# Performance work log

Hardware: AMD Instinct MI355X
Metric: run time of the kernel (lower is better)

Reference implementation:

```python
import jax, jax.numpy as jnp
import numpy as np

NUM_HEADS = 16
D_MODEL = 1024
D_KV = 64
NUM_BUCKETS = 32
MAX_DISTANCE = 128


def _relative_position_bucket(relative_position, num_buckets=NUM_BUCKETS, max_distance=MAX_DISTANCE):
    # faithful port of the torch static method (bidirectional variant)
    n = -relative_position
    nb = num_buckets // 2
    ret = (n < 0).astype(jnp.int32) * nb
    n = jnp.abs(n)
    max_exact = nb // 2
    is_small = n < max_exact
    # guard log(0); is_small branch covers n < max_exact anyway
    val_if_large = max_exact + (
        jnp.log(jnp.maximum(n, 1).astype(jnp.float32) / max_exact)
        / np.log(max_distance / max_exact)
        * (nb - max_exact)
    ).astype(jnp.int32)
    val_if_large = jnp.minimum(val_if_large, nb - 1)
    return ret + jnp.where(is_small, n, val_if_large)


def _compute_bias(seq_len, rel_bias):
    ctx = jnp.arange(seq_len)[:, None]
    mem = jnp.arange(seq_len)[None, :]
    bucket = _relative_position_bucket(mem - ctx)  # [S, S]
    values = rel_bias[bucket]                      # [S, S, H]
    return jnp.transpose(values, (2, 0, 1))[None]  # [1, H, S, S]


def setup_inputs() -> dict:
    key = jax.random.key(0)
    ks = jax.random.split(key, 6)
    B, S = 4, 1024
    scale = 1.0 / np.sqrt(D_MODEL)
    return {
        "hidden_states": jax.random.normal(ks[0], (B, S, D_MODEL), jnp.float32),
        "attention_mask": jnp.ones((B, 1, 1, S), jnp.int32),
        "Wq": jax.random.normal(ks[1], (NUM_HEADS * D_KV, D_MODEL), jnp.float32) * scale,
        "Wk": jax.random.normal(ks[2], (NUM_HEADS * D_KV, D_MODEL), jnp.float32) * scale,
        "Wv": jax.random.normal(ks[3], (NUM_HEADS * D_KV, D_MODEL), jnp.float32) * scale,
        "Wo": jax.random.normal(ks[4], (D_MODEL, NUM_HEADS * D_KV), jnp.float32) * scale,
        "rel_bias": jax.random.normal(ks[5], (NUM_BUCKETS, NUM_HEADS), jnp.float32),
    }


def reference(hidden_states, attention_mask, Wq, Wk, Wv, Wo, rel_bias):
    B, S, _ = hidden_states.shape
    # projections (Linear with bias=False: x @ W.T), reshape to [B, S, H, d_kv]
    q = jnp.einsum('bsd,ed->bse', hidden_states, Wq).reshape(B, S, NUM_HEADS, D_KV)
    k = jnp.einsum('bsd,ed->bse', hidden_states, Wk).reshape(B, S, NUM_HEADS, D_KV)
    v = jnp.einsum('bsd,ed->bse', hidden_states, Wv).reshape(B, S, NUM_HEADS, D_KV)
    scores = jnp.einsum('bqhd,bkhd->bhqk', q, k) / np.sqrt(D_KV)
    scores = scores + _compute_bias(S, rel_bias)
    scores = jnp.where(attention_mask == 0, jnp.float32(-1e9), scores)
    attn_weights = jax.nn.softmax(scores, axis=-1)  # dropout is identity at eval
    attn_output = jnp.einsum('bhqk,bkhd->bqhd', attn_weights, v).reshape(B, S, NUM_HEADS * D_KV)
    output = jnp.einsum('bse,de->bsd', attn_output, Wo)
    return output, attn_weights
```

## Files before the change

### kernel.cpp

```cpp
#include <hip/hip_runtime.h>
#include <hip/hip_bf16.h>

#define BB 4
#define SS 1024
#define HH 16
#define DK 64
#define DM 1024
#define MM (BB * SS)

typedef __attribute__((ext_vector_type(8))) short bh8_t;
typedef __attribute__((ext_vector_type(4))) float f4_t;

#define MFMA(a, b, c) __builtin_amdgcn_mfma_f32_16x16x32_bf16(a, b, c, 0, 0, 0)

__device__ __forceinline__ short f2bf(float f) {
    unsigned u = __builtin_bit_cast(unsigned, f);
    u = (u + 0x7FFFu + ((u >> 16) & 1u)) >> 16;
    return (short)u;
}
__device__ __forceinline__ float bf2f(short h) {
    unsigned u = ((unsigned)(unsigned short)h) << 16;
    return __builtin_bit_cast(float, u);
}

__device__ __forceinline__ int rel_bucket(int rel) {
    int n = -rel;
    int ret = 0;
    if (n < 0) { ret = 16; n = -n; }
    int v;
    if (n < 8) {
        v = n;
    } else {
        float t = logf((float)n * 0.125f) / 2.7725887298583984f * 8.0f;
        v = 8 + (int)t;
        if (v > 15) v = 15;
    }
    return ret + v;
}

__global__ __launch_bounds__(256)
void k_proj_qk(const float* __restrict__ X, const float* __restrict__ Wq,
               const float* __restrict__ Wk,
               short* __restrict__ Qh, short* __restrict__ Ql,
               short* __restrict__ Kh, short* __restrict__ Kl) {
    const int z = blockIdx.z;
    const float* W = z ? Wk : Wq;
    short* Oh = z ? Kh : Qh;
    short* Ol = z ? Kl : Ql;

    __shared__ short Ah[128][40], Al[128][40], Bh[128][40], Bl[128][40];

    const int tid = threadIdx.x;
    const int m0 = blockIdx.y * 128, n0 = blockIdx.x * 128;
    const int wave = tid >> 6, lane = tid & 63;
    const int quad = lane >> 4, lm = lane & 15;
    const int wm = (wave >> 1) * 64, wn = (wave & 1) * 64;
    const int r = tid >> 1, sg = (tid & 1) * 16;

    f4_t acc[4][4];
#pragma unroll
    for (int i = 0; i < 4; ++i)
#pragma unroll
        for (int j = 0; j < 4; ++j) acc[i][j] = (f4_t){0.f, 0.f, 0.f, 0.f};

    for (int k0 = 0; k0 < DM; k0 += 32) {
        f4_t xa[4], wb[4];
#pragma unroll
        for (int u = 0; u < 4; ++u) {
            xa[u] = *(const f4_t*)(X + (size_t)(m0 + r) * DM + k0 + sg + u * 4);
            wb[u] = *(const f4_t*)(W + (size_t)(n0 + r) * DM + k0 + sg + u * 4);
        }
        __syncthreads();
#pragma unroll
        for (int u = 0; u < 4; ++u) {
            short4 hh, ll;
            hh.x = f2bf(xa[u][0]); ll.x = f2bf(xa[u][0] - bf2f(hh.x));
            hh.y = f2bf(xa[u][1]); ll.y = f2bf(xa[u][1] - bf2f(hh.y));
            hh.z = f2bf(xa[u][2]); ll.z = f2bf(xa[u][2] - bf2f(hh.z));
            hh.w = f2bf(xa[u][3]); ll.w = f2bf(xa[u][3] - bf2f(hh.w));
            *(short4*)&Ah[r][sg + u * 4] = hh;
            *(short4*)&Al[r][sg + u * 4] = ll;
            hh.x = f2bf(wb[u][0]); ll.x = f2bf(wb[u][0] - bf2f(hh.x));
            hh.y = f2bf(wb[u][1]); ll.y = f2bf(wb[u][1] - bf2f(hh.y));
            hh.z = f2bf(wb[u][2]); ll.z = f2bf(wb[u][2] - bf2f(hh.z));
            hh.w = f2bf(wb[u][3]); ll.w = f2bf(wb[u][3] - bf2f(hh.w));
            *(short4*)&Bh[r][sg + u * 4] = hh;
            *(short4*)&Bl[r][sg + u * 4] = ll;
        }
        __syncthreads();

        bh8_t ah[4], al[4];
#pragma unroll
        for (int i = 0; i < 4; ++i) {
            ah[i] = *(const bh8_t*)&Ah[wm + i * 16 + lm][quad * 8];
            al[i] = *(const bh8_t*)&Al[wm + i * 16 + lm][quad * 8];
        }
#pragma unroll
        for (int j = 0; j < 4; ++j) {
            bh8_t bhj = *(const bh8_t*)&Bh[wn + j * 16 + lm][quad * 8];
            bh8_t blj = *(const bh8_t*)&Bl[wn + j * 16 + lm][quad * 8];
#pragma unroll
            for (int i = 0; i < 4; ++i) {
                acc[i][j] = MFMA(al[i], bhj, acc[i][j]);
                acc[i][j] = MFMA(ah[i], blj, acc[i][j]);
                acc[i][j] = MFMA(ah[i], bhj, acc[i][j]);
            }
        }
    }

#pragma unroll
    for (int i = 0; i < 4; ++i)
#pragma unroll
        for (int j = 0; j < 4; ++j)
#pragma unroll
            for (int g = 0; g < 4; ++g) {
                const int row = m0 + wm + i * 16 + quad * 4 + g;
                const int col = n0 + wn + j * 16 + lm;
                const int b = row >> 10, s = row & 1023;
                const int hd = col >> 6, dk = col & 63;
                const float v = acc[i][j][g];
                const short vh = f2bf(v);
                const short vl = f2bf(v - bf2f(vh));
                const size_t o = ((size_t)((b * HH + hd) * SS + s)) * DK + dk;
                Oh[o] = vh;
                Ol[o] = vl;
            }
}

__global__ __launch_bounds__(256)
void k_proj_v(const float* __restrict__ X, const float* __restrict__ Wv,
              short* __restrict__ Vt) {
    __shared__ short As[128][40], Bs[128][40];

    const int tid = threadIdx.x;
    const int m0 = blockIdx.y * 128, n0 = blockIdx.x * 128;
    const int wave = tid >> 6, lane = tid & 63;
    const int quad = lane >> 4, lm = lane & 15;
    const int wm = (wave >> 1) * 64, wn = (wave & 1) * 64;
    const int r = tid >> 1, sg = (tid & 1) * 16;

    f4_t acc[4][4];
#pragma unroll
    for (int i = 0; i < 4; ++i)
#pragma unroll
        for (int j = 0; j < 4; ++j) acc[i][j] = (f4_t){0.f, 0.f, 0.f, 0.f};

    for (int k0 = 0; k0 < DM; k0 += 32) {
        f4_t xa[4], wb[4];
#pragma unroll
        for (int u = 0; u < 4; ++u) {
            xa[u] = *(const f4_t*)(X + (size_t)(m0 + r) * DM + k0 + sg + u * 4);
            wb[u] = *(const f4_t*)(Wv + (size_t)(n0 + r) * DM + k0 + sg + u * 4);
        }
        __syncthreads();
#pragma unroll
        for (int u = 0; u < 4; ++u) {
            short4 hh;
            hh.x = f2bf(xa[u][0]); hh.y = f2bf(xa[u][1]);
            hh.z = f2bf(xa[u][2]); hh.w = f2bf(xa[u][3]);
            *(short4*)&As[r][sg + u * 4] = hh;
            hh.x = f2bf(wb[u][0]); hh.y = f2bf(wb[u][1]);
            hh.z = f2bf(wb[u][2]); hh.w = f2bf(wb[u][3]);
            *(short4*)&Bs[r][sg + u * 4] = hh;
        }
        __syncthreads();

        bh8_t ah[4];
#pragma unroll
        for (int i = 0; i < 4; ++i)
            ah[i] = *(const bh8_t*)&As[wm + i * 16 + lm][quad * 8];
#pragma unroll
        for (int j = 0; j < 4; ++j) {
            bh8_t bhj = *(const bh8_t*)&Bs[wn + j * 16 + lm][quad * 8];
#pragma unroll
            for (int i = 0; i < 4; ++i) acc[i][j] = MFMA(ah[i], bhj, acc[i][j]);
        }
    }

#pragma unroll
    for (int i = 0; i < 4; ++i)
#pragma unroll
        for (int j = 0; j < 4; ++j)
#pragma unroll
            for (int g = 0; g < 4; ++g) {
                const int row = m0 + wm + i * 16 + quad * 4 + g;
                const int col = n0 + wn + j * 16 + lm;
                const int b = row >> 10, s = row & 1023;
                const int hd = col >> 6, dk = col & 63;
                Vt[((size_t)((b * HH + hd) * DK + dk)) * SS + s] = f2bf(acc[i][j][g]);
            }
}

__global__ __launch_bounds__(256)
void k_scores(const short* __restrict__ Qh, const short* __restrict__ Ql,
              const short* __restrict__ Kh, const short* __restrict__ Kl,
              const int* __restrict__ mask, const float* __restrict__ rb,
              float* __restrict__ P) {
    __shared__ short Qhs[128][72], Qls[128][72], Khs[128][72], Kls[128][72];
    __shared__ float biasS[256];
    __shared__ int maskS[128];

    const int bh = blockIdx.z, b = bh >> 4, hd = bh & 15;
    const int q0 = blockIdx.y * 128, k0 = blockIdx.x * 128;
    const int tid = threadIdx.x;
    const int wave = tid >> 6, lane = tid & 63;
    const int quad = lane >> 4, lm = lane & 15;
    const int wm = (wave >> 1) * 64, wn = (wave & 1) * 64;

    {
        const int r = tid >> 1, sg = (tid & 1) * 32;
        const size_t qo = ((size_t)bh * SS + q0 + r) * DK + sg;
        const size_t ko = ((size_t)bh * SS + k0 + r) * DK + sg;
#pragma unroll
        for (int u = 0; u < 4; ++u) {
            *(uint4*)&Qhs[r][sg + u * 8] = *(const uint4*)(Qh + qo + u * 8);
            *(uint4*)&Qls[r][sg + u * 8] = *(const uint4*)(Ql + qo + u * 8);
            *(uint4*)&Khs[r][sg + u * 8] = *(const uint4*)(Kh + ko + u * 8);
            *(uint4*)&Kls[r][sg + u * 8] = *(const uint4*)(Kl + ko + u * 8);
        }
    }
    if (tid < 255) biasS[tid] = rb[rel_bucket(k0 - q0 + tid - 127) * HH + hd];
    if (tid < 128) maskS[tid] = mask[b * SS + k0 + tid];
    __syncthreads();

    f4_t acc[4][4];
#pragma unroll
    for (int i = 0; i < 4; ++i)
#pragma unroll
        for (int j = 0; j < 4; ++j) acc[i][j] = (f4_t){0.f, 0.f, 0.f, 0.f};

#pragma unroll
    for (int ks = 0; ks < 2; ++ks) {
        bh8_t ah[4], al[4];
#pragma unroll
        for (int i = 0; i < 4; ++i) {
            ah[i] = *(const bh8_t*)&Qhs[wm + i * 16 + lm][ks * 32 + quad * 8];
            al[i] = *(const bh8_t*)&Qls[wm + i * 16 + lm][ks * 32 + quad * 8];
        }
#pragma unroll
        for (int j = 0; j < 4; ++j) {
            bh8_t bhj = *(const bh8_t*)&Khs[wn + j * 16 + lm][ks * 32 + quad * 8];
            bh8_t blj = *(const bh8_t*)&Kls[wn + j * 16 + lm][ks * 32 + quad * 8];
#pragma unroll
            for (int i = 0; i < 4; ++i) {
                acc[i][j] = MFMA(al[i], bhj, acc[i][j]);
                acc[i][j] = MFMA(ah[i], blj, acc[i][j]);
                acc[i][j] = MFMA(ah[i], bhj, acc[i][j]);
            }
        }
    }

#pragma unroll
    for (int i = 0; i < 4; ++i)
#pragma unroll
        for (int j = 0; j < 4; ++j)
#pragma unroll
            for (int g = 0; g < 4; ++g) {
                const int rowl = wm + i * 16 + quad * 4 + g;
                const int coll = wn + j * 16 + lm;
                float s = acc[i][j][g] * 0.125f + biasS[coll - rowl + 127];
                s = (maskS[coll] == 0) ? -1e9f : s;
                P[((size_t)bh * SS + q0 + rowl) * SS + k0 + coll] = s;
            }
}

__global__ __launch_bounds__(256)
void k_softmax(float* __restrict__ P) {
    const size_t row = blockIdx.x;
    float4* p = reinterpret_cast<float4*>(P + row * 1024);
    const int tid = threadIdx.x;
    float4 v = p[tid];

    float m = fmaxf(fmaxf(v.x, v.y), fmaxf(v.z, v.w));
#pragma unroll
    for (int off = 32; off > 0; off >>= 1) m = fmaxf(m, __shfl_xor(m, off, 64));

    __shared__ float redm[4], reds[4];
    const int wave = tid >> 6, lane = tid & 63;
    if (lane == 0) redm[wave] = m;
    __syncthreads();
    m = fmaxf(fmaxf(redm[0], redm[1]), fmaxf(redm[2], redm[3]));

    const float e0 = expf(v.x - m), e1 = expf(v.y - m);
    const float e2 = expf(v.z - m), e3 = expf(v.w - m);
    float ssum = e0 + e1 + e2 + e3;
#pragma unroll
    for (int off = 32; off > 0; off >>= 1) ssum += __shfl_xor(ssum, off, 64);
    if (lane == 0) reds[wave] = ssum;
    __syncthreads();
    ssum = reds[0] + reds[1] + reds[2] + reds[3];

    const float inv = 1.0f / ssum;
    p[tid] = make_float4(e0 * inv, e1 * inv, e2 * inv, e3 * inv);
}

__global__ __launch_bounds__(256)
void k_pv(const float* __restrict__ P, const short* __restrict__ Vt,
          short* __restrict__ AO) {
    __shared__ short As[128][40];
    __shared__ short Bs[64][40];

    const int bh = blockIdx.y, b = bh >> 4, hd = bh & 15;
    const int q0 = blockIdx.x * 128;
    const int tid = threadIdx.x;
    const int wave = tid >> 6, lane = tid & 63;
    const int quad = lane >> 4, lm = lane & 15;
    const int wm = wave * 32;
    const int rA = tid >> 1, sgA = (tid & 1) * 16;
    const int rB = tid >> 2, sgB = (tid & 3) * 8;

    f4_t acc[2][4];
#pragma unroll
    for (int i = 0; i < 2; ++i)
#pragma unroll
        for (int j = 0; j < 4; ++j) acc[i][j] = (f4_t){0.f, 0.f, 0.f, 0.f};

    for (int k0 = 0; k0 < SS; k0 += 32) {
        f4_t pr[4];
#pragma unroll
        for (int u = 0; u < 4; ++u)
            pr[u] = *(const f4_t*)(P + ((size_t)bh * SS + q0 + rA) * SS + k0 + sgA + u * 4);
        uint4 vb = *(const uint4*)(Vt + ((size_t)bh * DK + rB) * SS + k0 + sgB);
        __syncthreads();
#pragma unroll
        for (int u = 0; u < 4; ++u) {
            short4 hh;
            hh.x = f2bf(pr[u][0]); hh.y = f2bf(pr[u][1]);
            hh.z = f2bf(pr[u][2]); hh.w = f2bf(pr[u][3]);
            *(short4*)&As[rA][sgA + u * 4] = hh;
        }
        *(uint4*)&Bs[rB][sgB] = vb;
        __syncthreads();

        bh8_t af0 = *(const bh8_t*)&As[wm + lm][quad * 8];
        bh8_t af1 = *(const bh8_t*)&As[wm + 16 + lm][quad * 8];
#pragma unroll
        for (int j = 0; j < 4; ++j) {
            bh8_t bf = *(const bh8_t*)&Bs[j * 16 + lm][quad * 8];
            acc[0][j] = MFMA(af0, bf, acc[0][j]);
            acc[1][j] = MFMA(af1, bf, acc[1][j]);
        }
    }

#pragma unroll
    for (int i = 0; i < 2; ++i)
#pragma unroll
        for (int j = 0; j < 4; ++j)
#pragma unroll
            for (int g = 0; g < 4; ++g) {
                const int s = q0 + wm + i * 16 + quad * 4 + g;
                const int dk = j * 16 + lm;
                AO[((size_t)(b * SS + s)) * DM + hd * DK + dk] = f2bf(acc[i][j][g]);
            }
}

__global__ __launch_bounds__(256)
void k_out(const short* __restrict__ A, const float* __restrict__ Wo,
           float* __restrict__ Out) {
    __shared__ short As[128][40], Bs[128][40];

    const int tid = threadIdx.x;
    const int m0 = blockIdx.y * 128, n0 = blockIdx.x * 128;
    const int wave = tid >> 6, lane = tid & 63;
    const int quad = lane >> 4, lm = lane & 15;
    const int wm = (wave >> 1) * 64, wn = (wave & 1) * 64;
    const int r = tid >> 1, sg = (tid & 1) * 16;

    f4_t acc[4][4];
#pragma unroll
    for (int i = 0; i < 4; ++i)
#pragma unroll
        for (int j = 0; j < 4; ++j) acc[i][j] = (f4_t){0.f, 0.f, 0.f, 0.f};

    for (int k0 = 0; k0 < DM; k0 += 32) {
        uint4 a0 = *(const uint4*)(A + (size_t)(m0 + r) * DM + k0 + sg);
        uint4 a1 = *(const uint4*)(A + (size_t)(m0 + r) * DM + k0 + sg + 8);
        f4_t wb[4];
#pragma unroll
        for (int u = 0; u < 4; ++u)
            wb[u] = *(const f4_t*)(Wo + (size_t)(n0 + r) * DM + k0 + sg + u * 4);
        __syncthreads();
        *(uint4*)&As[r][sg] = a0;
        *(uint4*)&As[r][sg + 8] = a1;
#pragma unroll
        for (int u = 0; u < 4; ++u) {
            short4 hh;
            hh.x = f2bf(wb[u][0]); hh.y = f2bf(wb[u][1]);
            hh.z = f2bf(wb[u][2]); hh.w = f2bf(wb[u][3]);
            *(short4*)&Bs[r][sg + u * 4] = hh;
        }
        __syncthreads();

        bh8_t ah[4];
#pragma unroll
        for (int i = 0; i < 4; ++i)
            ah[i] = *(const bh8_t*)&As[wm + i * 16 + lm][quad * 8];
#pragma unroll
        for (int j = 0; j < 4; ++j) {
            bh8_t bhj = *(const bh8_t*)&Bs[wn + j * 16 + lm][quad * 8];
#pragma unroll
            for (int i = 0; i < 4; ++i) acc[i][j] = MFMA(ah[i], bhj, acc[i][j]);
        }
    }

#pragma unroll
    for (int i = 0; i < 4; ++i)
#pragma unroll
        for (int j = 0; j < 4; ++j)
#pragma unroll
            for (int g = 0; g < 4; ++g)
                Out[(size_t)(m0 + wm + i * 16 + quad * 4 + g) * DM + n0 + wn + j * 16 + lm] =
                    acc[i][j][g];
}

extern "C" void kernel_launch(void* const* d_in, const int* in_sizes, int n_in,
                              void* d_out, int out_size, void* d_ws, size_t ws_size,
                              hipStream_t stream) {
    const float* X    = (const float*)d_in[0];
    const int*   mask = (const int*)d_in[1];
    const float* Wq   = (const float*)d_in[2];
    const float* Wk   = (const float*)d_in[3];
    const float* Wv   = (const float*)d_in[4];
    const float* Wo   = (const float*)d_in[5];
    const float* rb   = (const float*)d_in[6];

    float* out = (float*)d_out;
    float* P   = out + (size_t)BB * SS * DM;

    short* ws = (short*)d_ws;
    short* Qh = ws;
    short* Ql = ws + (size_t)4194304;
    short* Kh = ws + (size_t)8388608;
    short* Kl = ws + (size_t)12582912;
    short* Vt = ws + (size_t)16777216;
    short* AO = ws;

    k_proj_qk<<<dim3(8, 32, 2), 256, 0, stream>>>(X, Wq, Wk, Qh, Ql, Kh, Kl);
    k_proj_v <<<dim3(8, 32, 1), 256, 0, stream>>>(X, Wv, Vt);
    k_scores <<<dim3(8, 8, BB * HH), 256, 0, stream>>>(Qh, Ql, Kh, Kl, mask, rb, P);
    k_softmax<<<dim3(BB * HH * SS), 256, 0, stream>>>(P);
    k_pv     <<<dim3(8, BB * HH), 256, 0, stream>>>(P, Vt, AO);
    k_out    <<<dim3(8, 32), 256, 0, stream>>>(AO, Wo, out);
}
```

Before: 659.2 us.

## Pre-convert inputs to bf16 once and fuse scores with softmax

Adds a conversion kernel that turns X and all weights into bf16 hi/lo splits once, so the projection and output GEMMs load ready-made bf16 tiles instead of converting fp32 inside every K-loop. It also merges the score and softmax kernels: each block computes a full 16x1024 row strip of scores and normalises it in registers before writing P. This drops one full write-and-read of the 256 MB score matrix, at the cost of larger workspace traffic for the converted copies and lower per-block reuse of Q.

```diff
diff --git a/kernel.cpp b/kernel.cpp
--- a/kernel.cpp
+++ b/kernel.cpp
@@ -39,12 +39,44 @@
 }
 
 __global__ __launch_bounds__(256)
-void k_proj_qk(const float* __restrict__ X, const float* __restrict__ Wq,
-               const float* __restrict__ Wk,
+void k_cvt(const float* __restrict__ X, const float* __restrict__ Wq,
+           const float* __restrict__ Wk, const float* __restrict__ Wv,
+           const float* __restrict__ Wo,
+           short* __restrict__ Xh, short* __restrict__ Xl,
+           short* __restrict__ Wqh, short* __restrict__ Wql,
+           short* __restrict__ Wkh, short* __restrict__ Wkl,
+           short* __restrict__ Wvh, short* __restrict__ Woh) {
+    const long base = ((long)blockIdx.x * 256 + threadIdx.x) * 4;
+    const float* src;
+    short* dh;
+    short* dl = nullptr;
+    long off;
+    if (base < 4194304L)      { src = X;  dh = Xh;  dl = Xl;  off = base; }
+    else if (base < 5242880L) { src = Wq; dh = Wqh; dl = Wql; off = base - 4194304L; }
+    else if (base < 6291456L) { src = Wk; dh = Wkh; dl = Wkl; off = base - 5242880L; }
+    else if (base < 7340032L) { src = Wv; dh = Wvh;           off = base - 6291456L; }
+    else                      { src = Wo; dh = Woh;           off = base - 7340032L; }
+    float4 v = *(const float4*)(src + off);
+    short4 h;
+    h.x = f2bf(v.x); h.y = f2bf(v.y); h.z = f2bf(v.z); h.w = f2bf(v.w);
+    *(short4*)(dh + off) = h;
+    if (dl) {
+        short4 l;
+        l.x = f2bf(v.x - bf2f(h.x)); l.y = f2bf(v.y - bf2f(h.y));
+        l.z = f2bf(v.z - bf2f(h.z)); l.w = f2bf(v.w - bf2f(h.w));
+        *(short4*)(dl + off) = l;
+    }
+}
+
+__global__ __launch_bounds__(256)
+void k_proj_qk(const short* __restrict__ Xh, const short* __restrict__ Xl,
+               const short* __restrict__ Wqh, const short* __restrict__ Wql,
+               const short* __restrict__ Wkh, const short* __restrict__ Wkl,
                short* __restrict__ Qh, short* __restrict__ Ql,
                short* __restrict__ Kh, short* __restrict__ Kl) {
     const int z = blockIdx.z;
-    const float* W = z ? Wk : Wq;
+    const short* Wh_ = z ? Wkh : Wqh;
+    const short* Wl_ = z ? Wkl : Wql;
     short* Oh = z ? Kh : Qh;
     short* Ol = z ? Kl : Ql;
 
@@ -64,29 +96,17 @@
         for (int j = 0; j < 4; ++j) acc[i][j] = (f4_t){0.f, 0.f, 0.f, 0.f};
 
     for (int k0 = 0; k0 < DM; k0 += 32) {
-        f4_t xa[4], wb[4];
-#pragma unroll
-        for (int u = 0; u < 4; ++u) {
-            xa[u] = *(const f4_t*)(X + (size_t)(m0 + r) * DM + k0 + sg + u * 4);
-            wb[u] = *(const f4_t*)(W + (size_t)(n0 + r) * DM + k0 + sg + u * 4);
-        }
-        __syncthreads();
-#pragma unroll
-        for (int u = 0; u < 4; ++u) {
-            short4 hh, ll;
-            hh.x = f2bf(xa[u][0]); ll.x = f2bf(xa[u][0] - bf2f(hh.x));
-            hh.y = f2bf(xa[u][1]); ll.y = f2bf(xa[u][1] - bf2f(hh.y));
-            hh.z = f2bf(xa[u][2]); ll.z = f2bf(xa[u][2] - bf2f(hh.z));
-            hh.w = f2bf(xa[u][3]); ll.w = f2bf(xa[u][3] - bf2f(hh.w));
-            *(short4*)&Ah[r][sg + u * 4] = hh;
-            *(short4*)&Al[r][sg + u * 4] = ll;
-            hh.x = f2bf(wb[u][0]); ll.x = f2bf(wb[u][0] - bf2f(hh.x));
-            hh.y = f2bf(wb[u][1]); ll.y = f2bf(wb[u][1] - bf2f(hh.y));
-            hh.z = f2bf(wb[u][2]); ll.z = f2bf(wb[u][2] - bf2f(hh.z));
-            hh.w = f2bf(wb[u][3]); ll.w = f2bf(wb[u][3] - bf2f(hh.w));
-            *(short4*)&Bh[r][sg + u * 4] = hh;
-            *(short4*)&Bl[r][sg + u * 4] = ll;
-        }
+        const size_t ao = (size_t)(m0 + r) * DM + k0 + sg;
+        const size_t bo = (size_t)(n0 + r) * DM + k0 + sg;
+        uint4 ah0 = *(const uint4*)(Xh + ao), ah1 = *(const uint4*)(Xh + ao + 8);
+        uint4 al0 = *(const uint4*)(Xl + ao), al1 = *(const uint4*)(Xl + ao + 8);
+        uint4 bh0 = *(const uint4*)(Wh_ + bo), bh1 = *(const uint4*)(Wh_ + bo + 8);
+        uint4 bl0 = *(const uint4*)(Wl_ + bo), bl1 = *(const uint4*)(Wl_ + bo + 8);
+        __syncthreads();
+        *(uint4*)&Ah[r][sg] = ah0; *(uint4*)&Ah[r][sg + 8] = ah1;
+        *(uint4*)&Al[r][sg] = al0; *(uint4*)&Al[r][sg + 8] = al1;
+        *(uint4*)&Bh[r][sg] = bh0; *(uint4*)&Bh[r][sg + 8] = bh1;
+        *(uint4*)&Bl[r][sg] = bl0; *(uint4*)&Bl[r][sg + 8] = bl1;
         __syncthreads();
 
         bh8_t ah[4], al[4];
@@ -128,7 +148,7 @@
 }
 
 __global__ __launch_bounds__(256)
-void k_proj_v(const float* __restrict__ X, const float* __restrict__ Wv,
+void k_proj_v(const short* __restrict__ Xh, const short* __restrict__ Wvh,
               short* __restrict__ Vt) {
     __shared__ short As[128][40], Bs[128][40];
 
@@ -146,23 +166,13 @@
         for (int j = 0; j < 4; ++j) acc[i][j] = (f4_t){0.f, 0.f, 0.f, 0.f};
 
     for (int k0 = 0; k0 < DM; k0 += 32) {
-        f4_t xa[4], wb[4];
-#pragma unroll
-        for (int u = 0; u < 4; ++u) {
-            xa[u] = *(const f4_t*)(X + (size_t)(m0 + r) * DM + k0 + sg + u * 4);
-            wb[u] = *(const f4_t*)(Wv + (size_t)(n0 + r) * DM + k0 + sg + u * 4);
-        }
-        __syncthreads();
-#pragma unroll
-        for (int u = 0; u < 4; ++u) {
-            short4 hh;
-            hh.x = f2bf(xa[u][0]); hh.y = f2bf(xa[u][1]);
-            hh.z = f2bf(xa[u][2]); hh.w = f2bf(xa[u][3]);
-            *(short4*)&As[r][sg + u * 4] = hh;
-            hh.x = f2bf(wb[u][0]); hh.y = f2bf(wb[u][1]);
-            hh.z = f2bf(wb[u][2]); hh.w = f2bf(wb[u][3]);
-            *(short4*)&Bs[r][sg + u * 4] = hh;
-        }
+        const size_t ao = (size_t)(m0 + r) * DM + k0 + sg;
+        const size_t bo = (size_t)(n0 + r) * DM + k0 + sg;
+        uint4 a0 = *(const uint4*)(Xh + ao), a1 = *(const uint4*)(Xh + ao + 8);
+        uint4 b0 = *(const uint4*)(Wvh + bo), b1 = *(const uint4*)(Wvh + bo + 8);
+        __syncthreads();
+        *(uint4*)&As[r][sg] = a0; *(uint4*)&As[r][sg + 8] = a1;
+        *(uint4*)&Bs[r][sg] = b0; *(uint4*)&Bs[r][sg + 8] = b1;
         __syncthreads();
 
         bh8_t ah[4];
@@ -192,106 +202,141 @@
 }
 
 __global__ __launch_bounds__(256)
-void k_scores(const short* __restrict__ Qh, const short* __restrict__ Ql,
-              const short* __restrict__ Kh, const short* __restrict__ Kl,
-              const int* __restrict__ mask, const float* __restrict__ rb,
-              float* __restrict__ P) {
-    __shared__ short Qhs[128][72], Qls[128][72], Khs[128][72], Kls[128][72];
-    __shared__ float biasS[256];
-    __shared__ int maskS[128];
-
-    const int bh = blockIdx.z, b = bh >> 4, hd = bh & 15;
-    const int q0 = blockIdx.y * 128, k0 = blockIdx.x * 128;
+void k_ssm(const short* __restrict__ Qh, const short* __restrict__ Ql,
+           const short* __restrict__ Kh, const short* __restrict__ Kl,
+           const int* __restrict__ mask, const float* __restrict__ rb,
+           float* __restrict__ P) {
+    __shared__ short Qhs[16][72], Qls[16][72];
+    __shared__ short Khs[128][72], Kls[128][72];
+    __shared__ float biasS[1040];
+    __shared__ int maskS[1024];
+    __shared__ float red[4][16];
+
+    const int bh = blockIdx.y, b = bh >> 4, h = bh & 15;
+    const int q0 = blockIdx.x * 16;
     const int tid = threadIdx.x;
     const int wave = tid >> 6, lane = tid & 63;
     const int quad = lane >> 4, lm = lane & 15;
-    const int wm = (wave >> 1) * 64, wn = (wave & 1) * 64;
-
-    {
-        const int r = tid >> 1, sg = (tid & 1) * 32;
+
+    if (tid < 128) {
+        const int r = tid >> 3, sg = (tid & 7) * 8;
         const size_t qo = ((size_t)bh * SS + q0 + r) * DK + sg;
-        const size_t ko = ((size_t)bh * SS + k0 + r) * DK + sg;
+        *(uint4*)&Qhs[r][sg] = *(const uint4*)(Qh + qo);
+        *(uint4*)&Qls[r][sg] = *(const uint4*)(Ql + qo);
+    }
+    for (int i = tid; i < 1039; i += 256)
+        biasS[i] = rb[rel_bucket(i - 15 - q0) * HH + h];
+    *(int4*)&maskS[tid * 4] = *(const int4*)(mask + b * SS + tid * 4);
+    __syncthreads();
+
+    bh8_t qh[2], ql[2];
+#pragma unroll
+    for (int ks = 0; ks < 2; ++ks) {
+        qh[ks] = *(const bh8_t*)&Qhs[lm][ks * 32 + quad * 8];
+        ql[ks] = *(const bh8_t*)&Qls[lm][ks * 32 + quad * 8];
+    }
+
+    f4_t acc[16];
+#pragma unroll
+    for (int i = 0; i < 16; ++i) acc[i] = (f4_t){0.f, 0.f, 0.f, 0.f};
+
+    const int rK = tid >> 1, sgK = (tid & 1) * 32;
+#pragma unroll
+    for (int c = 0; c < 8; ++c) {
+        const int kc = c * 128;
+        uint4 vh[4], vl[4];
+        const size_t ko = ((size_t)bh * SS + kc + rK) * DK + sgK;
 #pragma unroll
         for (int u = 0; u < 4; ++u) {
-            *(uint4*)&Qhs[r][sg + u * 8] = *(const uint4*)(Qh + qo + u * 8);
-            *(uint4*)&Qls[r][sg + u * 8] = *(const uint4*)(Ql + qo + u * 8);
-            *(uint4*)&Khs[r][sg + u * 8] = *(const uint4*)(Kh + ko + u * 8);
-            *(uint4*)&Kls[r][sg + u * 8] = *(const uint4*)(Kl + ko + u * 8);
-        }
-    }
-    if (tid < 255) biasS[tid] = rb[rel_bucket(k0 - q0 + tid - 127) * HH + hd];
-    if (tid < 128) maskS[tid] = mask[b * SS + k0 + tid];
+            vh[u] = *(const uint4*)(Kh + ko + u * 8);
+            vl[u] = *(const uint4*)(Kl + ko + u * 8);
+        }
+        __syncthreads();
+#pragma unroll
+        for (int u = 0; u < 4; ++u) {
+            *(uint4*)&Khs[rK][sgK + u * 8] = vh[u];
+            *(uint4*)&Kls[rK][sgK + u * 8] = vl[u];
+        }
+        __syncthreads();
+
+#pragma unroll
+        for (int t = 0; t < 2; ++t) {
+            const int col0 = wave * 32 + t * 16;
+            const int ai = c * 2 + t;
+#pragma unroll
+            for (int ks = 0; ks < 2; ++ks) {
+                bh8_t kbh = *(const bh8_t*)&Khs[col0 + lm][ks * 32 + quad * 8];
+                bh8_t kbl = *(const bh8_t*)&Kls[col0 + lm][ks * 32 + quad * 8];
+                acc[ai] = MFMA(ql[ks], kbh, acc[ai]);
+                acc[ai] = MFMA(qh[ks], kbl, acc[ai]);
+                acc[ai] = MFMA(qh[ks], kbh, acc[ai]);
+            }
+        }
+    }
+
+#pragma unroll
+    for (int ai = 0; ai < 16; ++ai) {
+        const int colg = (ai >> 1) * 128 + wave * 32 + (ai & 1) * 16 + lm;
+        const int msk = maskS[colg];
+#pragma unroll
+        for (int g = 0; g < 4; ++g) {
+            const int row = quad * 4 + g;
+            float s = acc[ai][g] * 0.125f + biasS[colg - row + 15];
+            acc[ai][g] = (msk == 0) ? -1e9f : s;
+        }
+    }
+
+    float m[4];
+#pragma unroll
+    for (int g = 0; g < 4; ++g) {
+        m[g] = acc[0][g];
+#pragma unroll
+        for (int ai = 1; ai < 16; ++ai) m[g] = fmaxf(m[g], acc[ai][g]);
+#pragma unroll
+        for (int off = 1; off < 16; off <<= 1)
+            m[g] = fmaxf(m[g], __shfl_xor(m[g], off, 64));
+    }
+    if (lm == 0)
+#pragma unroll
+        for (int g = 0; g < 4; ++g) red[wave][quad * 4 + g] = m[g];
     __syncthreads();
-
-    f4_t acc[4][4];
-#pragma unroll
-    for (int i = 0; i < 4; ++i)
-#pragma unroll
-        for (int j = 0; j < 4; ++j) acc[i][j] = (f4_t){0.f, 0.f, 0.f, 0.f};
-
-#pragma unroll
-    for (int ks = 0; ks < 2; ++ks) {
-        bh8_t ah[4], al[4];
-#pragma unroll
-        for (int i = 0; i < 4; ++i) {
-            ah[i] = *(const bh8_t*)&Qhs[wm + i * 16 + lm][ks * 32 + quad * 8];
-            al[i] = *(const bh8_t*)&Qls[wm + i * 16 + lm][ks * 32 + quad * 8];
-        }
-#pragma unroll
-        for (int j = 0; j < 4; ++j) {
-            bh8_t bhj = *(const bh8_t*)&Khs[wn + j * 16 + lm][ks * 32 + quad * 8];
-            bh8_t blj = *(const bh8_t*)&Kls[wn + j * 16 + lm][ks * 32 + quad * 8];
-#pragma unroll
-            for (int i = 0; i < 4; ++i) {
-                acc[i][j] = MFMA(al[i], bhj, acc[i][j]);
-                acc[i][j] = MFMA(ah[i], blj, acc[i][j]);
-                acc[i][j] = MFMA(ah[i], bhj, acc[i][j]);
-            }
-        }
-    }
-
-#pragma unroll
-    for (int i = 0; i < 4; ++i)
-#pragma unroll
-        for (int j = 0; j < 4; ++j)
-#pragma unroll
-            for (int g = 0; g < 4; ++g) {
-                const int rowl = wm + i * 16 + quad * 4 + g;
-                const int coll = wn + j * 16 + lm;
-                float s = acc[i][j][g] * 0.125f + biasS[coll - rowl + 127];
-                s = (maskS[coll] == 0) ? -1e9f : s;
-                P[((size_t)bh * SS + q0 + rowl) * SS + k0 + coll] = s;
-            }
-}
-
-__global__ __launch_bounds__(256)
-void k_softmax(float* __restrict__ P) {
-    const size_t row = blockIdx.x;
-    float4* p = reinterpret_cast<float4*>(P + row * 1024);
-    const int tid = threadIdx.x;
-    float4 v = p[tid];
-
-    float m = fmaxf(fmaxf(v.x, v.y), fmaxf(v.z, v.w));
-#pragma unroll
-    for (int off = 32; off > 0; off >>= 1) m = fmaxf(m, __shfl_xor(m, off, 64));
-
-    __shared__ float redm[4], reds[4];
-    const int wave = tid >> 6, lane = tid & 63;
-    if (lane == 0) redm[wave] = m;
+#pragma unroll
+    for (int g = 0; g < 4; ++g)
+        m[g] = fmaxf(fmaxf(red[0][quad * 4 + g], red[1][quad * 4 + g]),
+                     fmaxf(red[2][quad * 4 + g], red[3][quad * 4 + g]));
     __syncthreads();
-    m = fmaxf(fmaxf(redm[0], redm[1]), fmaxf(redm[2], redm[3]));
-
-    const float e0 = expf(v.x - m), e1 = expf(v.y - m);
-    const float e2 = expf(v.z - m), e3 = expf(v.w - m);
-    float ssum = e0 + e1 + e2 + e3;
-#pragma unroll
-    for (int off = 32; off > 0; off >>= 1) ssum += __shfl_xor(ssum, off, 64);
-    if (lane == 0) reds[wave] = ssum;
+
+    float sum[4] = {0.f, 0.f, 0.f, 0.f};
+#pragma unroll
+    for (int ai = 0; ai < 16; ++ai)
+#pragma unroll
+        for (int g = 0; g < 4; ++g) {
+            const float e = __expf(acc[ai][g] - m[g]);
+            acc[ai][g] = e;
+            sum[g] += e;
+        }
+#pragma unroll
+    for (int g = 0; g < 4; ++g)
+#pragma unroll
+        for (int off = 1; off < 16; off <<= 1)
+            sum[g] += __shfl_xor(sum[g], off, 64);
+    if (lm == 0)
+#pragma unroll
+        for (int g = 0; g < 4; ++g) red[wave][quad * 4 + g] = sum[g];
     __syncthreads();
-    ssum = reds[0] + reds[1] + reds[2] + reds[3];
-
-    const float inv = 1.0f / ssum;
-    p[tid] = make_float4(e0 * inv, e1 * inv, e2 * inv, e3 * inv);
+    float inv[4];
+#pragma unroll
+    for (int g = 0; g < 4; ++g)
+        inv[g] = 1.0f / (red[0][quad * 4 + g] + red[1][quad * 4 + g] +
+                         red[2][quad * 4 + g] + red[3][quad * 4 + g]);
+
+#pragma unroll
+    for (int ai = 0; ai < 16; ++ai) {
+        const int colg = (ai >> 1) * 128 + wave * 32 + (ai & 1) * 16 + lm;
+#pragma unroll
+        for (int g = 0; g < 4; ++g)
+            P[((size_t)bh * SS + q0 + quad * 4 + g) * SS + colg] = acc[ai][g] * inv[g];
+    }
 }
 
 __global__ __launch_bounds__(256)
@@ -355,7 +400,7 @@
 }
 
 __global__ __launch_bounds__(256)
-void k_out(const short* __restrict__ A, const float* __restrict__ Wo,
+void k_out(const short* __restrict__ A, const short* __restrict__ Woh,
            float* __restrict__ Out) {
     __shared__ short As[128][40], Bs[128][40];
 
@@ -373,22 +418,13 @@
         for (int j = 0; j < 4; ++j) acc[i][j] = (f4_t){0.f, 0.f, 0.f, 0.f};
 
     for (int k0 = 0; k0 < DM; k0 += 32) {
-        uint4 a0 = *(const uint4*)(A + (size_t)(m0 + r) * DM + k0 + sg);
-        uint4 a1 = *(const uint4*)(A + (size_t)(m0 + r) * DM + k0 + sg + 8);
-        f4_t wb[4];
-#pragma unroll
-        for (int u = 0; u < 4; ++u)
-            wb[u] = *(const f4_t*)(Wo + (size_t)(n0 + r) * DM + k0 + sg + u * 4);
-        __syncthreads();
-        *(uint4*)&As[r][sg] = a0;
-        *(uint4*)&As[r][sg + 8] = a1;
-#pragma unroll
-        for (int u = 0; u < 4; ++u) {
-            short4 hh;
-            hh.x = f2bf(wb[u][0]); hh.y = f2bf(wb[u][1]);
-            hh.z = f2bf(wb[u][2]); hh.w = f2bf(wb[u][3]);
-            *(short4*)&Bs[r][sg + u * 4] = hh;
-        }
+        const size_t ao = (size_t)(m0 + r) * DM + k0 + sg;
+        const size_t bo = (size_t)(n0 + r) * DM + k0 + sg;
+        uint4 a0 = *(const uint4*)(A + ao), a1 = *(const uint4*)(A + ao + 8);
+        uint4 b0 = *(const uint4*)(Woh + bo), b1 = *(const uint4*)(Woh + bo + 8);
+        __syncthreads();
+        *(uint4*)&As[r][sg] = a0; *(uint4*)&As[r][sg + 8] = a1;
+        *(uint4*)&Bs[r][sg] = b0; *(uint4*)&Bs[r][sg + 8] = b1;
         __syncthreads();
 
         bh8_t ah[4];
@@ -427,18 +463,28 @@
     float* out = (float*)d_out;
     float* P   = out + (size_t)BB * SS * DM;
 
-    short* ws = (short*)d_ws;
-    short* Qh = ws;
-    short* Ql = ws + (size_t)4194304;
-    short* Kh = ws + (size_t)8388608;
-    short* Kl = ws + (size_t)12582912;
-    short* Vt = ws + (size_t)16777216;
-    short* AO = ws;
-
-    k_proj_qk<<<dim3(8, 32, 2), 256, 0, stream>>>(X, Wq, Wk, Qh, Ql, Kh, Kl);
-    k_proj_v <<<dim3(8, 32, 1), 256, 0, stream>>>(X, Wv, Vt);
-    k_scores <<<dim3(8, 8, BB * HH), 256, 0, stream>>>(Qh, Ql, Kh, Kl, mask, rb, P);
-    k_softmax<<<dim3(BB * HH * SS), 256, 0, stream>>>(P);
-    k_pv     <<<dim3(8, BB * HH), 256, 0, stream>>>(P, Vt, AO);
-    k_out    <<<dim3(8, 32), 256, 0, stream>>>(AO, Wo, out);
-}
+    short* ws  = (short*)d_ws;
+    short* Qh  = ws;
+    short* Ql  = ws + 4194304L;
+    short* Kh  = ws + 8388608L;
+    short* Kl  = ws + 12582912L;
+    short* Vt  = ws + 16777216L;
+    short* Xh  = ws + 20971520L;
+    short* Xl  = ws + 25165824L;
+    short* Wqh = ws + 29360128L;
+    short* Wql = ws + 30408704L;
+    short* Wkh = ws + 31457280L;
+    short* Wkl = ws + 32505856L;
+    short* Wvh = ws + 33554432L;
+    short* Woh = ws + 34603008L;
+    short* AO  = ws;
+
+    k_cvt    <<<8192, 256, 0, stream>>>(X, Wq, Wk, Wv, Wo, Xh, Xl, Wqh, Wql,
+                                        Wkh, Wkl, Wvh, Woh);
+    k_proj_qk<<<dim3(8, 32, 2), 256, 0, stream>>>(Xh, Xl, Wqh, Wql, Wkh, Wkl,
+                                                  Qh, Ql, Kh, Kl);
+    k_proj_v <<<dim3(8, 32), 256, 0, stream>>>(Xh, Wvh, Vt);
+    k_ssm    <<<dim3(64, 64), 256, 0, stream>>>(Qh, Ql, Kh, Kl, mask, rb, P);
+    k_pv     <<<dim3(8, 64), 256, 0, stream>>>(P, Vt, AO);
+    k_out    <<<dim3(8, 32), 256, 0, stream>>>(AO, Woh, out);
+}
```

Result: slower. 872.2 us (+32.3%).
